# Optimization experiments

Hardware: AMD Instinct MI355X
Metric: run time of the kernel (lower is better)

## Reference

```python
import jax, jax.numpy as jnp
import numpy as np
from jax import lax

N = 2; C_IN = 256
H0, W0 = 100, 152
H1, W1 = 50, 76
DYN_CH = 34            # 4 init_offset + 4 bound_pt_offset + 18 semantic_pt_offset + 8 reg_aggr_attn
REG_CH = 4             # 4 boundary points x 1 channel each
NUM_CLASSES = 80
SEM_PTS = 9
CLS_CH = SEM_PTS * NUM_CLASSES
BOUND_PTS = 4
RATIO = 0.5            # LIMIT_BOUND_POINT_OFFSET_RATIO

_BASE = np.array([[1,0,0,0],[0,1,0,0],[0.5,0,0.5,0],
                  [0,0.5,0,0.5],[0,0,1,0],[0,0,0,1]], np.float32)
BOUND_MAT = jnp.asarray(_BASE[[0,3,2,1,4,3,2,5]])                      # (8,4) box -> cross-shaped 4 pts
SEM_MAT = jnp.asarray(_BASE[[0,1,0,3,0,5,2,1,2,3,2,5,4,1,4,3,4,5]])    # (18,4) box -> 3x3 pts
BOUND_OFF_IDX = jnp.array([1, 2, 5, 6])   # tangential coordinate channel of each boundary point
LOC_IDX = jnp.array([0, 3, 4, 7])         # box-side coordinate channel of each boundary point

def conv3x3(x, w, b):
    y = lax.conv_general_dilated(x, w, (1, 1), 'SAME',
                                 dimension_numbers=('NCHW', 'OIHW', 'NCHW'))
    return y + b[None, :, None, None]

def conv1x1(x, w):
    return jnp.einsum('oi,nihw->nohw', w[:, :, 0, 0], x)

def pred_collect(fmap, pts, point_num, reduce_points, bias=None):
    # Bilinearly sample per-point channel groups of fmap at dynamic point locations.
    # fmap: (N, P*c, Hm, Wm); pts: (N, 2P, H, W) with (x, y) pairs per point.
    Nb, C, Hm, Wm = fmap.shape
    P = point_num; c = C // P
    H, W = pts.shape[2], pts.shape[3]
    fm = fmap.reshape(Nb, P, c, Hm, Wm)
    pg = pts.reshape(Nb, P, 2, H, W)
    def sample(f, pt):  # f: (c, Hm, Wm), pt: (2, H, W)
        x = jnp.clip(pt[0], 0.0, Wm - 1.0)
        y = jnp.clip(pt[1], 0.0, Hm - 1.0)
        x0 = jnp.floor(x); y0 = jnp.floor(y)
        fx = x - x0; fy = y - y0
        x0i = x0.astype(jnp.int32); y0i = y0.astype(jnp.int32)
        x1i = jnp.minimum(x0i + 1, Wm - 1); y1i = jnp.minimum(y0i + 1, Hm - 1)
        v00 = f[:, y0i, x0i]; v01 = f[:, y0i, x1i]
        v10 = f[:, y1i, x0i]; v11 = f[:, y1i, x1i]
        return v00*(1-fx)*(1-fy) + v01*fx*(1-fy) + v10*(1-fx)*fy + v11*fx*fy
    vals = jax.vmap(jax.vmap(sample))(fm, pg)  # (N, P, c, H, W)
    if reduce_points:
        out = vals.sum(axis=1)
        if bias is not None:
            out = out + bias[None, :, None, None]
        return out
    return vals.reshape(Nb, P * c, H, W)

def head_forward(reg_feats, cls_feats, anchors, dyn_w, dyn_b, reg_w, cls_w, cls_b):
    reg_maps = [conv1x1(x, reg_w) for x in reg_feats]
    cls_maps = [conv1x1(x, cls_w) for x in cls_feats]
    cls_scores, coarse_boxes, reg_boxes = [], [], []
    for i, (reg_feat, anchor) in enumerate(zip(reg_feats, anchors)):
        Nb, _, H, W = reg_feat.shape
        pred = conv3x3(reg_feat, dyn_w, dyn_b)
        init_off, bpt_off, spt_off, attn = jnp.split(pred, [4, 8, 26], axis=1)
        coarse = anchor + init_off                                  # (N,4,H,W) = (x1,y1,x2,y2)
        # straight-through clamp of boundary-point tangential offsets to +-wh/2*ratio
        bpt_off = bpt_off.reshape(Nb, 2, 2, 1, H, W)
        wh = jnp.stack([coarse[:, 3] - coarse[:, 1],
                        coarse[:, 2] - coarse[:, 0]], axis=1) / 2 * RATIO  # (N,2,H,W) [h,w]
        thres = wh[:, None, :, None]                                # (N,1,2,1,H,W)
        extra = jnp.maximum(bpt_off - thres, 0.0) + jnp.minimum(bpt_off + thres, 0.0)
        bpt_off = (bpt_off - lax.stop_gradient(extra)).reshape(Nb, 4, H, W)
        bound_pt = lax.stop_gradient(jnp.einsum('oc,nchw->nohw', BOUND_MAT, coarse))
        bound_pt = bound_pt.at[:, BOUND_OFF_IDX].add(bpt_off)       # (N,8,H,W)
        bound_pt_loc = bound_pt[:, LOC_IDX]                         # (N,4,H,W)
        reg_val = pred_collect(reg_maps[i], bound_pt, BOUND_PTS, False)  # (N,4,H,W)
        if i > 0:
            attn_sm = jax.nn.softmax(attn.reshape(Nb, BOUND_PTS, 2, H, W), axis=2)
            reg_hi = reg_val.reshape(Nb, BOUND_PTS, 1, 1, H, W)
            reg_lo = pred_collect(reg_maps[i - 1], bound_pt * 2, BOUND_PTS, False)
            reg_lo = reg_lo.reshape(Nb, BOUND_PTS, 1, 1, H, W) * 0.5
            reg_val = (jnp.concatenate([reg_lo, reg_hi], axis=2)
                       * attn_sm[:, :, :, None]).sum(axis=2).reshape(Nb, -1, H, W)
        reg_box = (lax.stop_gradient(bound_pt_loc) + reg_val).reshape(Nb, 4, -1, H, W).mean(axis=2)
        sem_pt = lax.stop_gradient(jnp.einsum('oc,nchw->nohw', SEM_MAT, coarse)) + spt_off
        cls_score = pred_collect(cls_maps[i], sem_pt, SEM_PTS, True, cls_b)  # (N,80,H,W)
        cls_scores.append(cls_score); coarse_boxes.append(coarse); reg_boxes.append(reg_box)
    return cls_scores, coarse_boxes, reg_boxes

def make_anchor(H, W):
    gy, gx = jnp.meshgrid(jnp.arange(H, dtype=jnp.float32),
                          jnp.arange(W, dtype=jnp.float32), indexing='ij')
    a = jnp.stack([gx - 4.0, gy - 4.0, gx + 4.0, gy + 4.0], axis=0)
    return jnp.broadcast_to(a[None], (N, 4, H, W))

def setup_inputs() -> dict:
    key = jax.random.key(0)
    ks = jax.random.split(key, 7)
    return {
        "reg_feat0": jax.random.normal(ks[0], (N, C_IN, H0, W0), jnp.float32),
        "reg_feat1": jax.random.normal(ks[1], (N, C_IN, H1, W1), jnp.float32),
        "cls_feat0": jax.random.normal(ks[2], (N, C_IN, H0, W0), jnp.float32),
        "cls_feat1": jax.random.normal(ks[3], (N, C_IN, H1, W1), jnp.float32),
        "anchor0": make_anchor(H0, W0),
        "anchor1": make_anchor(H1, W1),
        "dyn_w": jax.random.normal(ks[4], (DYN_CH, C_IN, 3, 3), jnp.float32) * 0.01,
        "dyn_b": jnp.zeros((DYN_CH,), jnp.float32),
        "reg_w": jax.random.normal(ks[5], (REG_CH, C_IN, 1, 1), jnp.float32) * 0.05,
        "cls_w": jax.random.normal(ks[6], (CLS_CH, C_IN, 1, 1), jnp.float32) * 0.05,
        "cls_b": jnp.zeros((NUM_CLASSES,), jnp.float32),
    }

def reference(reg_feat0, reg_feat1, cls_feat0, cls_feat1, anchor0, anchor1,
              dyn_w, dyn_b, reg_w, cls_w, cls_b):
    cls_scores, coarse_boxes, reg_boxes = head_forward(
        [reg_feat0, reg_feat1], [cls_feat0, cls_feat1], [anchor0, anchor1],
        dyn_w, dyn_b, reg_w, cls_w, cls_b)
    return (*cls_scores, *coarse_boxes, *reg_boxes)
```

## Files before the change

### kernel.cpp

```cpp
#include <hip/hip_runtime.h>
#include <hip/hip_bf16.h>
#include <cstdint>

#define N_BATCH 2
#define C_IN 256
#define DYN_CH 34
#define CLS_CH 720
#define NUM_CLASSES 80
#define NCOMB 48

#define P0c 15200
#define P1c 3800
#define M0c 30400
#define M1c 7600
#define MT0c 119
#define MT1c 30
#define CT0c 475
#define CT1c 119

typedef __attribute__((ext_vector_type(8))) short short8;
typedef __attribute__((ext_vector_type(4))) float f32x4;

typedef const unsigned int __attribute__((address_space(1)))* gas1_t;
typedef unsigned int __attribute__((address_space(3)))* las3_t;

__device__ __forceinline__ void async_ld16(const void* g, void* l) {
  __builtin_amdgcn_global_load_lds((gas1_t)g, (las3_t)l, 16, 0, 0);
}

__global__ __launch_bounds__(256) void pack_feat(
    const float* __restrict__ cls0, const float* __restrict__ cls1,
    const float* __restrict__ reg0, const float* __restrict__ reg1,
    const float* __restrict__ cls_w, const float* __restrict__ dyn_w,
    const float* __restrict__ reg_w, __hip_bfloat16* __restrict__ a0,
    __hip_bfloat16* __restrict__ a1, __hip_bfloat16* __restrict__ r0,
    __hip_bfloat16* __restrict__ r1, __hip_bfloat16* __restrict__ bpack,
    __hip_bfloat16* __restrict__ wpack) {
  int b = blockIdx.x;
  if (b >= 2384) {
    b -= 2384;
    if (b < 90) {
      int u = b * 256 + threadIdx.x;
      if (u >= 9 * 32 * 80) return;
      int ntile = u / 2560;
      int rem = u % 2560;
      int kcg = rem / 80;
      int ochl = rem % 80;
      int och = ntile * 80 + ochl;
      const float* wr = cls_w + (size_t)och * C_IN + kcg * 8;
      __hip_bfloat16 tmp[8];
#pragma unroll
      for (int c = 0; c < 8; ++c) tmp[c] = __float2bfloat16(wr[c]);
      *(uint4*)(bpack + (size_t)u * 8) = *(const uint4*)tmp;
    } else {
      int u = (b - 90) * 256 + threadIdx.x;
      if (u >= 13824) return;
      int j = u / 768;
      int r = u % 768;
      int n = r / 16;
      int s = r % 16;
      int ku = j * 16 + (s ^ (n & 7));
      int k0 = ku * 8;
      int tap = k0 >> 8;
      int c0 = k0 & 255;
      __hip_bfloat16 tmp[8];
#pragma unroll
      for (int i = 0; i < 8; ++i) {
        int c = c0 + i;
        float v = 0.f;
        if (n < DYN_CH) v = dyn_w[((size_t)n * C_IN + c) * 9 + tap];
        else if (n < DYN_CH + 4 && tap == 4)
          v = reg_w[(size_t)(n - DYN_CH) * C_IN + c];
        tmp[i] = __float2bfloat16(v);
      }
      *(uint4*)(wpack + (size_t)u * 8) = *(const uint4*)tmp;
    }
    return;
  }
  int j = b & 7;
  int mtg = b >> 3;
  const float* src;
  __hip_bfloat16* dst;
  int P, Mtot, mtile;
  if (mtg < 119)      { src = cls0; dst = a0; P = P0c; Mtot = M0c; mtile = mtg; }
  else if (mtg < 149) { src = cls1; dst = a1; P = P1c; Mtot = M1c; mtile = mtg - 119; }
  else if (mtg < 268) { src = reg0; dst = r0; P = P0c; Mtot = M0c; mtile = mtg - 149; }
  else                { src = reg1; dst = r1; P = P1c; Mtot = M1c; mtile = mtg - 268; }
  int wave = threadIdx.x >> 6;
  int lane = threadIdx.x & 63;
  int kcg = j * 4 + wave;
  int c0 = kcg * 8;
  int m4 = mtile * 256 + lane * 4;
  uint4* du = (uint4*)dst + (size_t)mtile * 8192 + (size_t)kcg * 256 + lane * 4;
  if (m4 < Mtot) {
    int n = m4 / P;
    int p = m4 - n * P;
    const float* sp = src + ((size_t)n * C_IN + c0) * P + p;
    float4 f[8];
#pragma unroll
    for (int c = 0; c < 8; ++c) f[c] = *(const float4*)(sp + (size_t)c * P);
#pragma unroll
    for (int i = 0; i < 4; ++i) {
      union { uint4 u; __hip_bfloat16 h[8]; } o;
#pragma unroll
      for (int c = 0; c < 8; ++c) {
        float v = (i == 0) ? f[c].x : (i == 1) ? f[c].y : (i == 2) ? f[c].z : f[c].w;
        o.h[c] = __float2bfloat16(v);
      }
      du[i] = o.u;
    }
  } else {
    uint4 z = {0u, 0u, 0u, 0u};
#pragma unroll
    for (int i = 0; i < 4; ++i) du[i] = z;
  }
}

__global__ __launch_bounds__(512) void cls_gemm_mfma(
    const uint4* __restrict__ Ap0, const uint4* __restrict__ Ap1,
    const uint4* __restrict__ Bp, __hip_bfloat16* __restrict__ out0,
    __hip_bfloat16* __restrict__ out1) {
  __shared__ uint4 Bsh[2560];
  int bb = blockIdx.x;
  int g = bb & 7;
  int loc = bb >> 3;
  int lm = loc / 9;
  int ntile = loc - lm * 9;
  int mtile = g * 19 + lm;
  if (mtile >= MT0c + MT1c) return;
  int tid = threadIdx.x;
  int w = tid >> 6;
  int lane = tid & 63;
  int l15 = lane & 15;
  int kq = lane >> 4;

  const uint4* Ap;
  __hip_bfloat16* out;
  int Mtot;
  if (mtile < MT0c) { Ap = Ap0; out = out0; Mtot = M0c; }
  else              { mtile -= MT0c; Ap = Ap1; out = out1; Mtot = M1c; }

  const uint4* Ab = Ap + (size_t)mtile * 8192;
  const uint4* Bb = Bp + (size_t)ntile * 2560;

#pragma unroll
  for (int i = 0; i < 5; ++i)
    async_ld16(Bb + i * 512 + w * 64 + lane, &Bsh[i * 512 + w * 64]);
  __syncthreads();

  f32x4 acc[2][5];
#pragma unroll
  for (int i = 0; i < 2; ++i)
#pragma unroll
    for (int j = 0; j < 5; ++j) acc[i][j] = (f32x4)0.f;

  const uint4* Abase = Ab + kq * 256 + w * 32 + l15;
#pragma unroll 2
  for (int kb = 0; kb < 8; ++kb) {
    uint4 a[2];
#pragma unroll
    for (int mi = 0; mi < 2; ++mi) a[mi] = Abase[kb * 1024 + mi * 16];
    short8 b[5];
    const uint4* Br = &Bsh[kb * 320 + kq * 80 + l15];
#pragma unroll
    for (int ni = 0; ni < 5; ++ni) b[ni] = *(const short8*)&Br[ni * 16];
#pragma unroll
    for (int mi = 0; mi < 2; ++mi)
#pragma unroll
      for (int ni = 0; ni < 5; ++ni)
        acc[mi][ni] = __builtin_amdgcn_mfma_f32_16x16x32_bf16(
            b[ni], *(const short8*)&a[mi], acc[mi][ni], 0, 0, 0);
  }

  int gbase = mtile * 256 + w * 32;
#pragma unroll
  for (int mi = 0; mi < 2; ++mi) {
    int px = gbase + mi * 16 + l15;
    if (px >= Mtot) continue;
    __hip_bfloat16* orow = out + (size_t)px * CLS_CH + ntile * 80 + kq * 4;
#pragma unroll
    for (int ni = 0; ni < 5; ++ni) {
      union { uint2 u; __hip_bfloat16 h[4]; } o;
#pragma unroll
      for (int r = 0; r < 4; ++r) o.h[r] = __float2bfloat16(acc[mi][ni][r]);
      *(uint2*)(orow + ni * 16) = o.u;
    }
  }
}

__global__ __launch_bounds__(256) void dyn_reg_conv_mfma(
    const uint4* __restrict__ rp0, const uint4* __restrict__ rp1,
    const uint4* __restrict__ wp, float* __restrict__ part0,
    float* __restrict__ part1) {
  __shared__ uint4 Bs[768];
  int g = blockIdx.x & 7;
  int i = blockIdx.x >> 3;
  int cnt = 74 + (g < 2 ? 1 : 0);
  if (i >= cnt) return;
  int bx = g * 74 + (g < 2 ? g : 2) + i;
  int tid = threadIdx.x;
  int wave = tid >> 6;
  int lane = tid & 63;
  int l15 = lane & 15;
  int kq = lane >> 4;

  const uint4* rp;
  float* part;
  int Mtot, P, W, H;
  if (bx < CT0c) { rp = rp0; part = part0; Mtot = M0c; P = P0c; W = 152; H = 100; }
  else { bx -= CT0c; rp = rp1; part = part1; Mtot = M1c; P = P1c; W = 76; H = 50; }

  int m = bx * 64 + wave * 16 + l15;
  bool mval = (m < Mtot);
  int mc = mval ? m : 0;
  int n = mc / P;
  int rem = mc - n * P;
  int y = rem / W;
  int x = rem - y * W;

  f32x4 acc[3];
#pragma unroll
  for (int q = 0; q < 3; ++q) acc[q] = (f32x4)0.f;

  for (int j = 0; j < 18; ++j) {
    const uint4* wsrc = wp + (size_t)j * 768 + wave * 192;
#pragma unroll
    for (int q = 0; q < 3; ++q)
      async_ld16(wsrc + q * 64 + lane, &Bs[wave * 192 + q * 64]);

    int tap = j >> 1;
    int cb8 = (j & 1) * 16;
    int dy = tap / 3 - 1, dx = tap % 3 - 1;
    int sy = y + dy, sx = x + dx;
    bool val = mval && ((unsigned)sy < (unsigned)H) && ((unsigned)sx < (unsigned)W);
    int sm = m + dy * W + dx;
    int smc = val ? sm : 0;
    size_t tbase = (size_t)(smc >> 8) * 8192 + (smc & 255);
    uint4 a[4];
#pragma unroll
    for (int t = 0; t < 4; ++t) {
      uint4 v = {0u, 0u, 0u, 0u};
      if (val) v = rp[tbase + (size_t)(cb8 + t * 4 + kq) * 256];
      a[t] = v;
    }
    __syncthreads();
#pragma unroll
    for (int t = 0; t < 4; ++t) {
#pragma unroll
      for (int ni = 0; ni < 3; ++ni) {
        int nn = ni * 16 + l15;
        short8 bf = *(const short8*)&Bs[nn * 16 + ((t * 4 + kq) ^ (nn & 7))];
        acc[ni] = __builtin_amdgcn_mfma_f32_16x16x32_bf16(
            *(short8*)&a[t], bf, acc[ni], 0, 0, 0);
      }
    }
    __syncthreads();
  }

  int mrow = bx * 64 + wave * 16 + kq * 4;
#pragma unroll
  for (int r = 0; r < 4; ++r) {
    int mm = mrow + r;
    if (mm >= Mtot) continue;
    float* dst = part + (size_t)mm * NCOMB + l15;
#pragma unroll
    for (int ni = 0; ni < 3; ++ni) dst[ni * 16] = acc[ni][r];
  }
}

__device__ __forceinline__ float samp(const float* __restrict__ part,
                                      int nbase, int W, int H,
                                      float px, float py, int ch) {
  float xc = fminf(fmaxf(px, 0.f), (float)(W - 1));
  float yc = fminf(fmaxf(py, 0.f), (float)(H - 1));
  float x0f = floorf(xc), y0f = floorf(yc);
  float fx = xc - x0f, fy = yc - y0f;
  int x0 = (int)x0f, y0 = (int)y0f;
  int x1 = min(x0 + 1, W - 1), y1 = min(y0 + 1, H - 1);
  float v00 = part[(size_t)(nbase + y0 * W + x0) * NCOMB + ch];
  float v01 = part[(size_t)(nbase + y0 * W + x1) * NCOMB + ch];
  float v10 = part[(size_t)(nbase + y1 * W + x0) * NCOMB + ch];
  float v11 = part[(size_t)(nbase + y1 * W + x1) * NCOMB + ch];
  return v00 * (1.f - fx) * (1.f - fy) + v01 * fx * (1.f - fy) +
         v10 * (1.f - fx) * fy + v11 * fx * fy;
}

__global__ __launch_bounds__(256) void decode_gather(
    const float* __restrict__ part0, const float* __restrict__ part1,
    const float* __restrict__ dyn_b, const float* __restrict__ anchor0,
    const float* __restrict__ anchor1,
    const __hip_bfloat16* __restrict__ map0,
    const __hip_bfloat16* __restrict__ map1, const float* __restrict__ bias,
    float* __restrict__ out_coarse0, float* __restrict__ out_coarse1,
    float* __restrict__ out_regbox0, float* __restrict__ out_regbox1,
    float* __restrict__ outc0, float* __restrict__ outc1) {
  __shared__ int4 s_idx[9][64];
  __shared__ float4 s_wt[9][64];
  __shared__ float s_out[80][65];
  int g = blockIdx.x & 7;
  int ib = blockIdx.x >> 3;
  int cnt = 74 + (g < 2 ? 1 : 0);
  if (ib >= cnt) return;
  int u = g * 74 + (g < 2 ? g : 2) + ib;

  const float* part;
  const float* anchor;
  float* out_coarse;
  float* out_regbox;
  const __hip_bfloat16* map;
  float* outc;
  int Mtot, H, W, P, level, mbase;
  if (u < 475) {
    part = part0; anchor = anchor0; out_coarse = out_coarse0;
    out_regbox = out_regbox0; map = map0; outc = outc0;
    Mtot = M0c; H = 100; W = 152; P = P0c; level = 0; mbase = u * 64;
  } else {
    part = part1; anchor = anchor1; out_coarse = out_coarse1;
    out_regbox = out_regbox1; map = map1; outc = outc1;
    Mtot = M1c; H = 50; W = 76; P = P1c; level = 1; mbase = (u - 475) * 64;
  }
  int tid = threadIdx.x;
  int wv = tid >> 6;
  int lane = tid & 63;

  if (wv == 0) {
    int m = mbase + lane;
    if (m < Mtot) {
      int n = m / P;
      int p = m - n * P;
      float pr[40];
      {
        const float4* q0 = (const float4*)(part + (size_t)m * NCOMB);
#pragma unroll
        for (int o4 = 0; o4 < 10; ++o4) {
          float4 a = q0[o4];
          pr[4 * o4 + 0] = a.x;
          pr[4 * o4 + 1] = a.y;
          pr[4 * o4 + 2] = a.z;
          pr[4 * o4 + 3] = a.w;
        }
#pragma unroll
        for (int o = 0; o < DYN_CH; ++o) pr[o] += dyn_b[o];
      }
      const float* an = anchor + (size_t)n * 4 * P + p;
      float cb[4];
#pragma unroll
      for (int k = 0; k < 4; ++k) cb[k] = an[(size_t)k * P] + pr[k];
      float* oc = out_coarse + (size_t)n * 4 * P + p;
#pragma unroll
      for (int k = 0; k < 4; ++k) oc[(size_t)k * P] = cb[k];

      float thr_y = (cb[3] - cb[1]) * 0.25f;
      float thr_x = (cb[2] - cb[0]) * 0.25f;
      float bo[4];
#pragma unroll
      for (int j = 0; j < 4; ++j) {
        float thr = (j & 1) ? thr_x : thr_y;
        float b = pr[4 + j];
        float extra = fmaxf(b - thr, 0.f) + fminf(b + thr, 0.f);
        bo[j] = b - extra;
      }
      float cx = 0.5f * (cb[0] + cb[2]);
      float cy = 0.5f * (cb[1] + cb[3]);
      float bp[8] = {cb[0], cy + bo[0], cx + bo[1], cb[1],
                     cb[2], cy + bo[2], cx + bo[3], cb[3]};

      int nbase = n * P;
      int nbaseLo = n * P0c;
      float rb[4];
#pragma unroll
      for (int pt = 0; pt < 4; ++pt) {
        float hi = samp(part, nbase, W, H, bp[2 * pt], bp[2 * pt + 1],
                        DYN_CH + pt);
        float val;
        if (level == 0) {
          val = hi;
        } else {
          float lo = 0.5f * samp(part0, nbaseLo, 152, 100, bp[2 * pt] * 2.f,
                                 bp[2 * pt + 1] * 2.f, DYN_CH + pt);
          float e0 = pr[26 + 2 * pt], e1 = pr[26 + 2 * pt + 1];
          float mx = fmaxf(e0, e1);
          float w0 = expf(e0 - mx), w1 = expf(e1 - mx);
          val = (lo * w0 + hi * w1) / (w0 + w1);
        }
        rb[pt] = val;
      }
      float* orb = out_regbox + (size_t)n * 4 * P + p;
      orb[0] = bp[0] + rb[0];
      orb[(size_t)P] = bp[3] + rb[1];
      orb[(size_t)2 * P] = bp[4] + rb[2];
      orb[(size_t)3 * P] = bp[7] + rb[3];

      float sx[9] = {cb[0], cb[0], cb[0], cx, cx, cx, cb[2], cb[2], cb[2]};
      float sy[9] = {cb[1], cy, cb[3], cb[1], cy, cb[3], cb[1], cy, cb[3]};
#pragma unroll
      for (int k = 0; k < 9; ++k) {
        float px = sx[k] + pr[8 + 2 * k];
        float py = sy[k] + pr[8 + 2 * k + 1];
        float xc = fminf(fmaxf(px, 0.f), (float)(W - 1));
        float yc = fminf(fmaxf(py, 0.f), (float)(H - 1));
        float x0f = floorf(xc), y0f = floorf(yc);
        float fx = xc - x0f, fy = yc - y0f;
        int x0 = (int)x0f, y0 = (int)y0f;
        int x1 = min(x0 + 1, W - 1), y1 = min(y0 + 1, H - 1);
        int4 iv;
        iv.x = (nbase + y0 * W + x0) * CLS_CH + k * 80;
        iv.y = (x1 - x0) * CLS_CH;
        iv.z = (y1 - y0) * W * CLS_CH;
        iv.w = 0;
        s_idx[k][lane] = iv;
        float4 wv4 = {(1.f - fx) * (1.f - fy), fx * (1.f - fy),
                      (1.f - fx) * fy, fx * fy};
        s_wt[k][lane] = wv4;
      }
    }
  }
  __syncthreads();

  int sub = lane / 20;
  if (sub > 2) sub = 2;
  int cl = lane % 20;
  int c4 = cl * 4;
  for (int r = 0; r < 16; ++r) {
    int pxl = wv * 16 + r;
    int m = mbase + pxl;
    if (m >= Mtot) break;
    float a0 = 0.f, a1 = 0.f, a2 = 0.f, a3 = 0.f;
#pragma unroll
    for (int gg = 0; gg < 3; ++gg) {
      int pt = gg * 3 + sub;
      int4 iv = s_idx[pt][pxl];
      float4 wt = s_wt[pt][pxl];
      const __hip_bfloat16* pl = map + iv.x + c4;
      uint2 t00 = *(const uint2*)(pl);
      uint2 t01 = *(const uint2*)(pl + iv.y);
      uint2 t10 = *(const uint2*)(pl + iv.z);
      uint2 t11 = *(const uint2*)(pl + iv.y + iv.z);
      a0 += wt.x * __uint_as_float(t00.x << 16) +
            wt.y * __uint_as_float(t01.x << 16) +
            wt.z * __uint_as_float(t10.x << 16) +
            wt.w * __uint_as_float(t11.x << 16);
      a1 += wt.x * __uint_as_float(t00.x & 0xffff0000u) +
            wt.y * __uint_as_float(t01.x & 0xffff0000u) +
            wt.z * __uint_as_float(t10.x & 0xffff0000u) +
            wt.w * __uint_as_float(t11.x & 0xffff0000u);
      a2 += wt.x * __uint_as_float(t00.y << 16) +
            wt.y * __uint_as_float(t01.y << 16) +
            wt.z * __uint_as_float(t10.y << 16) +
            wt.w * __uint_as_float(t11.y << 16);
      a3 += wt.x * __uint_as_float(t00.y & 0xffff0000u) +
            wt.y * __uint_as_float(t01.y & 0xffff0000u) +
            wt.z * __uint_as_float(t10.y & 0xffff0000u) +
            wt.w * __uint_as_float(t11.y & 0xffff0000u);
    }
    {
      float s0 = __shfl(a0, lane + 20), u0 = __shfl(a0, lane + 40);
      float s1 = __shfl(a1, lane + 20), u1 = __shfl(a1, lane + 40);
      float s2 = __shfl(a2, lane + 20), u2 = __shfl(a2, lane + 40);
      float s3 = __shfl(a3, lane + 20), u3 = __shfl(a3, lane + 40);
      a0 += s0 + u0;
      a1 += s1 + u1;
      a2 += s2 + u2;
      a3 += s3 + u3;
    }
    if (lane < 20) {
      s_out[c4 + 0][pxl] = a0;
      s_out[c4 + 1][pxl] = a1;
      s_out[c4 + 2][pxl] = a2;
      s_out[c4 + 3][pxl] = a3;
    }
  }
  __syncthreads();

  for (int k = tid; k < 80 * 16; k += 256) {
    int c = k >> 4;
    int q = k & 15;
    int m4 = mbase + q * 4;
    if (m4 >= Mtot) continue;
    int n = m4 / P;
    int p4 = m4 - n * P;
    float bb = bias[c];
    float4 v = {s_out[c][q * 4 + 0] + bb, s_out[c][q * 4 + 1] + bb,
                s_out[c][q * 4 + 2] + bb, s_out[c][q * 4 + 3] + bb};
    *(float4*)&outc[((size_t)n * NUM_CLASSES + c) * P + p4] = v;
  }
}

extern "C" void kernel_launch(void* const* d_in, const int* in_sizes, int n_in,
                              void* d_out, int out_size, void* d_ws,
                              size_t ws_size, hipStream_t stream) {
  const float* reg_feat0 = (const float*)d_in[0];
  const float* reg_feat1 = (const float*)d_in[1];
  const float* cls_feat0 = (const float*)d_in[2];
  const float* cls_feat1 = (const float*)d_in[3];
  const float* anchor0 = (const float*)d_in[4];
  const float* anchor1 = (const float*)d_in[5];
  const float* dyn_w = (const float*)d_in[6];
  const float* dyn_b = (const float*)d_in[7];
  const float* reg_w = (const float*)d_in[8];
  const float* cls_w = (const float*)d_in[9];
  const float* cls_b = (const float*)d_in[10];

  float* out = (float*)d_out;
  float* out_cls0 = out;
  float* out_cls1 = out_cls0 + (size_t)N_BATCH * NUM_CLASSES * P0c;
  float* out_coarse0 = out_cls1 + (size_t)N_BATCH * NUM_CLASSES * P1c;
  float* out_coarse1 = out_coarse0 + (size_t)N_BATCH * 4 * P0c;
  float* out_reg0 = out_coarse1 + (size_t)N_BATCH * 4 * P1c;
  float* out_reg1 = out_reg0 + (size_t)N_BATCH * 4 * P0c;

  char* w = (char*)d_ws;
  __hip_bfloat16* bpack = (__hip_bfloat16*)w;   w += 368640;
  __hip_bfloat16* wpack = (__hip_bfloat16*)w;   w += 221184;
  __hip_bfloat16* apack0 = (__hip_bfloat16*)w;  w += 15597568;
  __hip_bfloat16* apack1 = (__hip_bfloat16*)w;  w += 3932160;
  __hip_bfloat16* rpack0 = (__hip_bfloat16*)w;  w += 15597568;
  __hip_bfloat16* rpack1 = (__hip_bfloat16*)w;  w += 3932160;
  float* part1 = (float*)w;                     w += 1459200;
  __hip_bfloat16* map0 = (__hip_bfloat16*)w;    w += 43776000;
  __hip_bfloat16* map1 = (__hip_bfloat16*)w;    w += 10944000;
  float* part0 = (float*)w;                     w += 5836800;

  hipLaunchKernelGGL(pack_feat, dim3(2528), dim3(256), 0, stream, cls_feat0,
                     cls_feat1, reg_feat0, reg_feat1, cls_w, dyn_w, reg_w,
                     apack0, apack1, rpack0, rpack1, bpack, wpack);
  hipLaunchKernelGGL(cls_gemm_mfma, dim3(8 * 19 * 9), dim3(512), 0, stream,
                     (const uint4*)apack0, (const uint4*)apack1,
                     (const uint4*)bpack, map0, map1);
  hipLaunchKernelGGL(dyn_reg_conv_mfma, dim3(600), dim3(256), 0,
                     stream, (const uint4*)rpack0, (const uint4*)rpack1,
                     (const uint4*)wpack, part0, part1);
  hipLaunchKernelGGL(decode_gather, dim3(600), dim3(256), 0, stream, part0,
                     part1, dyn_b, anchor0, anchor1, map0, map1, cls_b,
                     out_coarse0, out_coarse1, out_reg0, out_reg1, out_cls0,
                     out_cls1);
}
```

Measured before the change: 207.5 us.

## Overlap reg-feature packing with cls GEMM by fusing into one launch

Splits the packing kernel so only the cls features and cls weights are packed before the GEMM. Packing of the reg features and the dyn/reg weights moves into extra blocks of the cls GEMM kernel, so that memory-bound conversion work runs alongside MFMA work. This shortens the critical path of the first pack. In exchange, pack blocks now run at 512 threads and the LDS footprint is shared with the GEMM blocks.

```diff
diff --git a/kernel.cpp b/kernel.cpp
--- a/kernel.cpp
+++ b/kernel.cpp
@@ -28,32 +28,95 @@
   __builtin_amdgcn_global_load_lds((gas1_t)g, (las3_t)l, 16, 0, 0);
 }
 
-__global__ __launch_bounds__(256) void pack_feat(
+__device__ __forceinline__ void pack_unit(const float* __restrict__ src,
+                                          __hip_bfloat16* __restrict__ dst,
+                                          int P, int Mtot, int mtile, int kcg,
+                                          int lane) {
+  int c0 = kcg * 8;
+  int m4 = mtile * 256 + lane * 4;
+  uint4* du = (uint4*)dst + (size_t)mtile * 8192 + (size_t)kcg * 256 + lane * 4;
+  if (m4 < Mtot) {
+    int n = m4 / P;
+    int p = m4 - n * P;
+    const float* sp = src + ((size_t)n * C_IN + c0) * P + p;
+    float4 f[8];
+#pragma unroll
+    for (int c = 0; c < 8; ++c) f[c] = *(const float4*)(sp + (size_t)c * P);
+#pragma unroll
+    for (int i = 0; i < 4; ++i) {
+      union { uint4 u; __hip_bfloat16 h[8]; } o;
+#pragma unroll
+      for (int c = 0; c < 8; ++c) {
+        float v = (i == 0) ? f[c].x : (i == 1) ? f[c].y : (i == 2) ? f[c].z : f[c].w;
+        o.h[c] = __float2bfloat16(v);
+      }
+      du[i] = o.u;
+    }
+  } else {
+    uint4 z = {0u, 0u, 0u, 0u};
+#pragma unroll
+    for (int i = 0; i < 4; ++i) du[i] = z;
+  }
+}
+
+__global__ __launch_bounds__(256) void pack_cls(
     const float* __restrict__ cls0, const float* __restrict__ cls1,
-    const float* __restrict__ reg0, const float* __restrict__ reg1,
-    const float* __restrict__ cls_w, const float* __restrict__ dyn_w,
-    const float* __restrict__ reg_w, __hip_bfloat16* __restrict__ a0,
-    __hip_bfloat16* __restrict__ a1, __hip_bfloat16* __restrict__ r0,
-    __hip_bfloat16* __restrict__ r1, __hip_bfloat16* __restrict__ bpack,
-    __hip_bfloat16* __restrict__ wpack) {
+    const float* __restrict__ cls_w, __hip_bfloat16* __restrict__ a0,
+    __hip_bfloat16* __restrict__ a1, __hip_bfloat16* __restrict__ bpack) {
   int b = blockIdx.x;
-  if (b >= 2384) {
-    b -= 2384;
-    if (b < 90) {
-      int u = b * 256 + threadIdx.x;
-      if (u >= 9 * 32 * 80) return;
-      int ntile = u / 2560;
-      int rem = u % 2560;
-      int kcg = rem / 80;
-      int ochl = rem % 80;
-      int och = ntile * 80 + ochl;
-      const float* wr = cls_w + (size_t)och * C_IN + kcg * 8;
-      __hip_bfloat16 tmp[8];
-#pragma unroll
-      for (int c = 0; c < 8; ++c) tmp[c] = __float2bfloat16(wr[c]);
-      *(uint4*)(bpack + (size_t)u * 8) = *(const uint4*)tmp;
+  if (b >= 1192) {
+    int u = (b - 1192) * 256 + threadIdx.x;
+    if (u >= 9 * 32 * 80) return;
+    int ntile = u / 2560;
+    int rem = u % 2560;
+    int kcg = rem / 80;
+    int ochl = rem % 80;
+    int och = ntile * 80 + ochl;
+    const float* wr = cls_w + (size_t)och * C_IN + kcg * 8;
+    __hip_bfloat16 tmp[8];
+#pragma unroll
+    for (int c = 0; c < 8; ++c) tmp[c] = __float2bfloat16(wr[c]);
+    *(uint4*)(bpack + (size_t)u * 8) = *(const uint4*)tmp;
+    return;
+  }
+  int j = b & 7;
+  int mtg = b >> 3;
+  const float* src;
+  __hip_bfloat16* dst;
+  int P, Mtot, mtile;
+  if (mtg < 119) { src = cls0; dst = a0; P = P0c; Mtot = M0c; mtile = mtg; }
+  else           { src = cls1; dst = a1; P = P1c; Mtot = M1c; mtile = mtg - 119; }
+  int wave = threadIdx.x >> 6;
+  int lane = threadIdx.x & 63;
+  pack_unit(src, dst, P, Mtot, mtile, j * 4 + wave, lane);
+}
+
+__global__ __launch_bounds__(512) void gemm_pack_fused(
+    const uint4* __restrict__ Ap0, const uint4* __restrict__ Ap1,
+    const uint4* __restrict__ Bp, __hip_bfloat16* __restrict__ out0,
+    __hip_bfloat16* __restrict__ out1, const float* __restrict__ reg0,
+    const float* __restrict__ reg1, const float* __restrict__ dyn_w,
+    const float* __restrict__ reg_w, __hip_bfloat16* __restrict__ r0,
+    __hip_bfloat16* __restrict__ r1, __hip_bfloat16* __restrict__ wpack) {
+  __shared__ uint4 Bsh[2560];
+  int tid = threadIdx.x;
+  int w = tid >> 6;
+  int lane = tid & 63;
+
+  if (blockIdx.x >= 1368) {
+    int pk = blockIdx.x - 1368;
+    if (pk < 596) {
+      int mtg = pk >> 2;
+      int jp = pk & 3;
+      const float* src;
+      __hip_bfloat16* dst;
+      int P, Mtot, mtile;
+      if (mtg < 119) { src = reg0; dst = r0; P = P0c; Mtot = M0c; mtile = mtg; }
+      else           { src = reg1; dst = r1; P = P1c; Mtot = M1c; mtile = mtg - 119; }
+      int j = jp * 2 + (w >> 2);
+      pack_unit(src, dst, P, Mtot, mtile, j * 4 + (w & 3), lane);
     } else {
-      int u = (b - 90) * 256 + threadIdx.x;
+      int u = (pk - 596) * 512 + tid;
       if (u >= 13824) return;
       int j = u / 768;
       int r = u % 768;
@@ -77,50 +140,7 @@
     }
     return;
   }
-  int j = b & 7;
-  int mtg = b >> 3;
-  const float* src;
-  __hip_bfloat16* dst;
-  int P, Mtot, mtile;
-  if (mtg < 119)      { src = cls0; dst = a0; P = P0c; Mtot = M0c; mtile = mtg; }
-  else if (mtg < 149) { src = cls1; dst = a1; P = P1c; Mtot = M1c; mtile = mtg - 119; }
-  else if (mtg < 268) { src = reg0; dst = r0; P = P0c; Mtot = M0c; mtile = mtg - 149; }
-  else                { src = reg1; dst = r1; P = P1c; Mtot = M1c; mtile = mtg - 268; }
-  int wave = threadIdx.x >> 6;
-  int lane = threadIdx.x & 63;
-  int kcg = j * 4 + wave;
-  int c0 = kcg * 8;
-  int m4 = mtile * 256 + lane * 4;
-  uint4* du = (uint4*)dst + (size_t)mtile * 8192 + (size_t)kcg * 256 + lane * 4;
-  if (m4 < Mtot) {
-    int n = m4 / P;
-    int p = m4 - n * P;
-    const float* sp = src + ((size_t)n * C_IN + c0) * P + p;
-    float4 f[8];
-#pragma unroll
-    for (int c = 0; c < 8; ++c) f[c] = *(const float4*)(sp + (size_t)c * P);
-#pragma unroll
-    for (int i = 0; i < 4; ++i) {
-      union { uint4 u; __hip_bfloat16 h[8]; } o;
-#pragma unroll
-      for (int c = 0; c < 8; ++c) {
-        float v = (i == 0) ? f[c].x : (i == 1) ? f[c].y : (i == 2) ? f[c].z : f[c].w;
-        o.h[c] = __float2bfloat16(v);
-      }
-      du[i] = o.u;
-    }
-  } else {
-    uint4 z = {0u, 0u, 0u, 0u};
-#pragma unroll
-    for (int i = 0; i < 4; ++i) du[i] = z;
-  }
-}
-
-__global__ __launch_bounds__(512) void cls_gemm_mfma(
-    const uint4* __restrict__ Ap0, const uint4* __restrict__ Ap1,
-    const uint4* __restrict__ Bp, __hip_bfloat16* __restrict__ out0,
-    __hip_bfloat16* __restrict__ out1) {
-  __shared__ uint4 Bsh[2560];
+
   int bb = blockIdx.x;
   int g = bb & 7;
   int loc = bb >> 3;
@@ -128,9 +148,6 @@
   int ntile = loc - lm * 9;
   int mtile = g * 19 + lm;
   if (mtile >= MT0c + MT1c) return;
-  int tid = threadIdx.x;
-  int w = tid >> 6;
-  int lane = tid & 63;
   int l15 = lane & 15;
   int kq = lane >> 4;
 
@@ -521,12 +538,12 @@
   __hip_bfloat16* map1 = (__hip_bfloat16*)w;    w += 10944000;
   float* part0 = (float*)w;                     w += 5836800;
 
-  hipLaunchKernelGGL(pack_feat, dim3(2528), dim3(256), 0, stream, cls_feat0,
-                     cls_feat1, reg_feat0, reg_feat1, cls_w, dyn_w, reg_w,
-                     apack0, apack1, rpack0, rpack1, bpack, wpack);
-  hipLaunchKernelGGL(cls_gemm_mfma, dim3(8 * 19 * 9), dim3(512), 0, stream,
+  hipLaunchKernelGGL(pack_cls, dim3(1282), dim3(256), 0, stream, cls_feat0,
+                     cls_feat1, cls_w, apack0, apack1, bpack);
+  hipLaunchKernelGGL(gemm_pack_fused, dim3(1991), dim3(512), 0, stream,
                      (const uint4*)apack0, (const uint4*)apack1,
-                     (const uint4*)bpack, map0, map1);
+                     (const uint4*)bpack, map0, map1, reg_feat0, reg_feat1,
+                     dyn_w, reg_w, rpack0, rpack1, wpack);
   hipLaunchKernelGGL(dyn_reg_conv_mfma, dim3(600), dim3(256), 0,
                      stream, (const uint4*)rpack0, (const uint4*)rpack1,
                      (const uint4*)wpack, part0, part1);
```

Measured after the change: 209.8 us. Within noise of the previous version (+1.1%).
